# Performance work log

Hardware: AMD Instinct MI355X
Metric: run time of the kernel (lower is better)

Reference implementation:

```python
import jax, jax.numpy as jnp
import numpy as np

STRIDES = (8, 16, 32, 64, 128)
HS = (192, 96, 48, 24, 12)
NUM_CLASSES = 15
NUM_THETA = 18
B = 16
SCORE_THR = 0.05
IOU_THR = 0.3
MAX_DET = 1000


def setup_inputs() -> dict:
    key = jax.random.key(0)
    ks = jax.random.split(key, 20)
    inp = {}
    i = 0
    for name, c in (("cls", NUM_CLASSES), ("reg", 5), ("tc", NUM_THETA), ("tr", 1)):
        for l, h in enumerate(HS):
            inp[f"{name}_l{l}"] = jax.random.normal(ks[i], (B, c, h, h), dtype=jnp.float32)
            i += 1
    return inp


def _coords():
    # FCOS-style location centers per level, concatenated: [N, 2] (x, y)
    outs = []
    for h, s in zip(HS, STRIDES):
        c1d = jnp.arange(h, dtype=jnp.float32) * s + s // 2
        yy, xx = jnp.meshgrid(c1d, c1d, indexing="ij")
        outs.append(jnp.stack([xx.ravel(), yy.ravel()], axis=-1))
    return jnp.concatenate(outs, axis=0)


def _flatten(levels):
    # list of [B,C,h,w] -> [B, sum(h*w), C]  (permute to NHWC then reshape, as in torch)
    b = levels[0].shape[0]
    return jnp.concatenate(
        [jnp.transpose(t, (0, 2, 3, 1)).reshape(b, -1, t.shape[1]) for t in levels], axis=1
    )


def _pairwise_iou(boxes):
    # boxes [M,5] (x1,y1,x2,y2,theta); axis-aligned IoU on first 4 coords
    x1, y1, x2, y2 = boxes[:, 0], boxes[:, 1], boxes[:, 2], boxes[:, 3]
    area = jnp.clip(x2 - x1, 0.0) * jnp.clip(y2 - y1, 0.0)
    iw = jnp.clip(jnp.minimum(x2[:, None], x2[None, :]) - jnp.maximum(x1[:, None], x1[None, :]), 0.0)
    ih = jnp.clip(jnp.minimum(y2[:, None], y2[None, :]) - jnp.maximum(y1[:, None], y1[None, :]), 0.0)
    inter = iw * ih
    union = area[:, None] + area[None, :] - inter
    return inter / jnp.maximum(union, 1e-8)


def _nms_keep(boxes, valid, iou_thr):
    # greedy NMS over score-sorted boxes; returns bool keep mask [M]
    m = boxes.shape[0]
    iou = _pairwise_iou(boxes)
    idx = jnp.arange(m)

    def body(i, keep):
        sup = keep[i] & (iou[i] > iou_thr) & (idx > i)
        return keep & ~sup

    return jax.lax.fori_loop(0, m, body, valid)


def _forward(cls_levels, reg_levels, tc_levels, tr_levels):
    coords = _coords()  # [N,2]

    cls_preds = jax.nn.sigmoid(_flatten(cls_levels))          # [B,N,15]
    cls_scores = jnp.max(cls_preds, axis=-1)                   # [B,N]
    cls_classes = jnp.argmax(cls_preds, axis=-1) + 1           # [B,N]

    tc_preds = jax.nn.sigmoid(_flatten(tc_levels))             # [B,N,18]
    theta_c = (jnp.argmax(tc_preds, axis=-1) + 1)[..., None].astype(jnp.float32)  # [B,N,1]
    tr_lo = _flatten(tr_levels)                                # [B,N,1]
    theta = theta_c * 10.0 + tr_lo                             # [B,N,1]

    # reg: scale ltrb channels (0:4) by stride per level, keep angle channel raw
    reg_parts = []
    for t, s in zip(reg_levels, STRIDES):
        r = jnp.transpose(t, (0, 2, 3, 1)).reshape(t.shape[0], -1, 5)
        reg_parts.append(jnp.concatenate([r[..., :4] * float(s), r[..., 4:]], axis=-1))
    reg = jnp.concatenate(reg_parts, axis=1)                   # [B,N,5]

    x1y1 = coords[None, :, :] - reg[..., :2]
    x2y2 = coords[None, :, :] + reg[..., 2:4]
    boxes = jnp.concatenate([x1y1, x2y2, theta], axis=-1)      # [B,N,5]

    max_num = min(MAX_DET, cls_scores.shape[-1])
    top_scores, top_idx = jax.lax.top_k(cls_scores, max_num)   # sorted desc
    boxes_topk = jnp.take_along_axis(boxes, top_idx[..., None], axis=1)   # [B,M,5]
    classes_topk = jnp.take_along_axis(cls_classes, top_idx, axis=1)      # [B,M]

    valid = top_scores >= SCORE_THR
    keep = jax.vmap(lambda b, v: _nms_keep(b, v, IOU_THR))(boxes_topk, valid)  # [B,M] bool

    scores_post = top_scores * keep
    classes_post = classes_topk * keep
    boxes_post = boxes_topk * keep[..., None]
    return scores_post, classes_post, boxes_post


def reference(cls_l0, cls_l1, cls_l2, cls_l3, cls_l4,
              reg_l0, reg_l1, reg_l2, reg_l3, reg_l4,
              tc_l0, tc_l1, tc_l2, tc_l3, tc_l4,
              tr_l0, tr_l1, tr_l2, tr_l3, tr_l4):
    return _forward(
        [cls_l0, cls_l1, cls_l2, cls_l3, cls_l4],
        [reg_l0, reg_l1, reg_l2, reg_l3, reg_l4],
        [tc_l0, tc_l1, tc_l2, tc_l3, tc_l4],
        [tr_l0, tr_l1, tr_l2, tr_l3, tr_l4],
    )
```

## Files before the change

kernel.cpp:

```cpp
#include <hip/hip_runtime.h>
#include <stdint.h>

#define NCLS   15
#define NTH    18
#define BATCH  16
#define NANCH  49104
#define KTOP   1000
#define NWORDS 16
#define NBIN   32768
#define BSHIFT 15
#define CAND   2048

__device__ __forceinline__ float sigmoidf(float x) {
    return 1.0f / (1.0f + expf(-x));
}

__device__ __forceinline__ void levelOf(int i, int& lvl, int& h, int& s, int& pos) {
    if (i < 36864)      { lvl = 0; h = 192; s = 8;   pos = i; }
    else if (i < 46080) { lvl = 1; h = 96;  s = 16;  pos = i - 36864; }
    else if (i < 48384) { lvl = 2; h = 48;  s = 32;  pos = i - 46080; }
    else if (i < 48960) { lvl = 3; h = 24;  s = 64;  pos = i - 48384; }
    else                { lvl = 4; h = 12;  s = 128; pos = i - 48960; }
}

__device__ __forceinline__ unsigned long long shfl_u64(unsigned long long v, int src) {
    int lo = __shfl((int)(unsigned int)(v & 0xFFFFFFFFull), src);
    int hi = __shfl((int)(unsigned int)(v >> 32), src);
    return ((unsigned long long)(unsigned int)hi << 32) | (unsigned long long)(unsigned int)lo;
}

__device__ __forceinline__ void atomicOr64Shared(unsigned long long* p, unsigned long long v) {
    unsigned int* q = (unsigned int*)p;
    unsigned int lo = (unsigned int)v;
    unsigned int hi = (unsigned int)(v >> 32);
    if (lo) atomicOr(q, lo);
    if (hi) atomicOr(q + 1, hi);
}

__global__ __launch_bounds__(256) void k_scores(
    const float* __restrict__ c0, const float* __restrict__ c1,
    const float* __restrict__ c2, const float* __restrict__ c3,
    const float* __restrict__ c4,
    float* __restrict__ scores, unsigned int* __restrict__ hist)
{
    __shared__ unsigned int lh[NBIN / 2];
    const int b = blockIdx.y;
    for (int i = threadIdx.x; i < NBIN / 2; i += 256) lh[i] = 0u;
    __syncthreads();

    #pragma unroll
    for (int r = 0; r < 2; ++r) {
        int f4 = blockIdx.x * 512 + r * 256 + threadIdx.x;
        if (f4 < NANCH / 4) {
            int i = f4 * 4;
            int lvl, h, s, pos;
            levelOf(i, lvl, h, s, pos);
            int hh = h * h;
            const float* cp = (lvl == 0) ? c0 : (lvl == 1) ? c1 : (lvl == 2) ? c2
                              : (lvl == 3) ? c3 : c4;
            const float* base = cp + (size_t)b * NCLS * hh + pos;
            float4 mx = make_float4(-1e30f, -1e30f, -1e30f, -1e30f);
            #pragma unroll
            for (int c = 0; c < NCLS; ++c) {
                float4 v = *(const float4*)(base + (size_t)c * hh);
                mx.x = fmaxf(mx.x, v.x); mx.y = fmaxf(mx.y, v.y);
                mx.z = fmaxf(mx.z, v.z); mx.w = fmaxf(mx.w, v.w);
            }
            float4 sc = make_float4(sigmoidf(mx.x), sigmoidf(mx.y),
                                    sigmoidf(mx.z), sigmoidf(mx.w));
            *(float4*)(scores + (size_t)b * NANCH + i) = sc;
            unsigned int bin;
            bin = __float_as_uint(sc.x) >> BSHIFT;
            atomicAdd(&lh[bin >> 1], 1u << ((bin & 1) << 4));
            bin = __float_as_uint(sc.y) >> BSHIFT;
            atomicAdd(&lh[bin >> 1], 1u << ((bin & 1) << 4));
            bin = __float_as_uint(sc.z) >> BSHIFT;
            atomicAdd(&lh[bin >> 1], 1u << ((bin & 1) << 4));
            bin = __float_as_uint(sc.w) >> BSHIFT;
            atomicAdd(&lh[bin >> 1], 1u << ((bin & 1) << 4));
        }
    }
    __syncthreads();

    unsigned int* hb = hist + (size_t)b * NBIN;
    for (int wd = threadIdx.x; wd < NBIN / 2; wd += 256) {
        unsigned int v = lh[wd];
        if (v) {
            unsigned int lo = v & 0xFFFFu, hi = v >> 16;
            if (lo) atomicAdd(&hb[wd * 2], lo);
            if (hi) atomicAdd(&hb[wd * 2 + 1], hi);
        }
    }
}

__global__ __launch_bounds__(256) void k_findT(
    const unsigned int* __restrict__ hist, int* __restrict__ tbin)
{
    int b = blockIdx.x;
    int tid = threadIdx.x;
    const unsigned int* hb = hist + (size_t)b * NBIN;
    __shared__ unsigned int sc[256];
    __shared__ unsigned int fsc[128];
    __shared__ int s_c, s_t;

    unsigned int s = 0;
    const uint4* hv = (const uint4*)(hb + (size_t)tid * 128);
    #pragma unroll 8
    for (int k = 0; k < 32; ++k) {
        uint4 v = hv[k];
        s += v.x + v.y + v.z + v.w;
    }
    sc[tid] = s;
    if (tid == 0) { s_c = 0; s_t = 0; }
    __syncthreads();
    for (int d = 1; d < 256; d <<= 1) {
        unsigned int add = (tid + d < 256) ? sc[tid + d] : 0;
        __syncthreads();
        sc[tid] += add;
        __syncthreads();
    }
    if (sc[tid] >= (unsigned int)KTOP && (tid == 255 || sc[tid + 1] < (unsigned int)KTOP))
        s_c = tid;
    __syncthreads();
    int c = s_c;
    unsigned int hi = (c < 255) ? sc[c + 1] : 0;
    if (tid < 128) fsc[tid] = hb[c * 128 + tid];
    __syncthreads();
    for (int d = 1; d < 128; d <<= 1) {
        unsigned int add = (tid < 128 && tid + d < 128) ? fsc[tid + d] : 0;
        __syncthreads();
        if (tid < 128) fsc[tid] += add;
        __syncthreads();
    }
    if (tid < 128 && hi + fsc[tid] >= (unsigned int)KTOP &&
        (tid == 127 || hi + fsc[tid + 1] < (unsigned int)KTOP))
        s_t = tid;
    __syncthreads();
    if (tid == 0) tbin[b] = c * 128 + s_t;
}

__global__ __launch_bounds__(256) void k_compact(
    const float* __restrict__ scores, const int* __restrict__ tbin,
    int* __restrict__ cnt, unsigned long long* __restrict__ cand)
{
    const int b = blockIdx.y;
    const int t4 = blockIdx.x * 256 + threadIdx.x;
    __shared__ int lcnt;
    __shared__ int lbase;
    if (threadIdx.x == 0) lcnt = 0;
    __syncthreads();

    const int T = tbin[b];
    const bool in = (t4 < NANCH / 4);
    float4 v = make_float4(0.f, 0.f, 0.f, 0.f);
    if (in) v = *(const float4*)(scores + (size_t)b * NANCH + 4 * (size_t)t4);
    unsigned int bits[4] = { __float_as_uint(v.x), __float_as_uint(v.y),
                             __float_as_uint(v.z), __float_as_uint(v.w) };
    int rank[4];
    #pragma unroll
    for (int k = 0; k < 4; ++k) {
        bool pass = in && ((int)(bits[k] >> BSHIFT) >= T);
        rank[k] = pass ? atomicAdd(&lcnt, 1) : -1;
    }
    __syncthreads();
    if (threadIdx.x == 0) lbase = atomicAdd(&cnt[b * 16], lcnt);
    __syncthreads();
    const int base = lbase;
    #pragma unroll
    for (int k = 0; k < 4; ++k) {
        if (rank[k] >= 0) {
            int p = base + rank[k];
            if (p < CAND) {
                unsigned int idx = 4u * (unsigned int)t4 + (unsigned int)k;
                cand[(size_t)b * CAND + p] =
                    ((unsigned long long)bits[k] << 32) |
                    (unsigned long long)(0xFFFFFFFFu - idx);
            }
        }
    }
}

__global__ __launch_bounds__(1024) void k_sortk(
    const unsigned long long* __restrict__ cand, const int* __restrict__ cnt,
    float* __restrict__ tsc, int* __restrict__ tix)
{
    int b = blockIdx.x;
    int tid = threadIdx.x;
    __shared__ unsigned long long keys[CAND];
    int n = cnt[b * 16]; if (n > CAND) n = CAND;
    for (int i = tid; i < CAND; i += 1024)
        keys[i] = (i < n) ? cand[(size_t)b * CAND + i] : 0ull;
    __syncthreads();
    for (int sz = 2; sz <= CAND; sz <<= 1) {
        for (int st = sz >> 1; st > 0; st >>= 1) {
            for (int i = tid; i < CAND; i += 1024) {
                int j = i ^ st;
                if (j > i) {
                    unsigned long long a = keys[i], c = keys[j];
                    bool desc = ((i & sz) == 0);
                    if (desc ? (a < c) : (a > c)) { keys[i] = c; keys[j] = a; }
                }
            }
            __syncthreads();
        }
    }
    if (tid < KTOP) {
        unsigned long long key = keys[tid];
        tsc[b * KTOP + tid] = __uint_as_float((unsigned int)(key >> 32));
        tix[b * KTOP + tid] = (int)(0xFFFFFFFFu - (unsigned int)(key & 0xFFFFFFFFull));
    }
}

__global__ __launch_bounds__(256) void k_decode(
    const float* __restrict__ c0, const float* __restrict__ c1,
    const float* __restrict__ c2, const float* __restrict__ c3,
    const float* __restrict__ c4,
    const float* __restrict__ r0, const float* __restrict__ r1,
    const float* __restrict__ r2, const float* __restrict__ r3,
    const float* __restrict__ r4,
    const float* __restrict__ t0, const float* __restrict__ t1,
    const float* __restrict__ t2, const float* __restrict__ t3,
    const float* __restrict__ t4,
    const float* __restrict__ q0, const float* __restrict__ q1,
    const float* __restrict__ q2, const float* __restrict__ q3,
    const float* __restrict__ q4,
    const int* __restrict__ tix, float* __restrict__ boxes, int* __restrict__ clstop)
{
    int g = blockIdx.x * 256 + threadIdx.x;
    if (g >= BATCH * KTOP) return;
    int b = g / KTOP;
    int idx = tix[g];
    int lvl, h, s, pos;
    levelOf(idx, lvl, h, s, pos);
    int y = pos / h, x = pos - y * h;
    int hh = h * h;
    const float* cp = (lvl == 0) ? c0 : (lvl == 1) ? c1 : (lvl == 2) ? c2 : (lvl == 3) ? c3 : c4;
    const float* rp = (lvl == 0) ? r0 : (lvl == 1) ? r1 : (lvl == 2) ? r2 : (lvl == 3) ? r3 : r4;
    const float* tp = (lvl == 0) ? t0 : (lvl == 1) ? t1 : (lvl == 2) ? t2 : (lvl == 3) ? t3 : t4;
    const float* qp = (lvl == 0) ? q0 : (lvl == 1) ? q1 : (lvl == 2) ? q2 : (lvl == 3) ? q3 : q4;
    int off = y * h + x;

    const float* cb = cp + (size_t)b * NCLS * hh + off;
    float bestc = -1e30f; int bc = 0;
    #pragma unroll
    for (int c = 0; c < NCLS; ++c) {
        float v = sigmoidf(cb[(size_t)c * hh]);
        if (v > bestc) { bestc = v; bc = c; }
    }
    clstop[g] = bc + 1;

    const float* tb = tp + (size_t)b * NTH * hh + off;
    float best = -1e30f; int bt = 0;
    #pragma unroll
    for (int c = 0; c < NTH; ++c) {
        float v = sigmoidf(tb[(size_t)c * hh]);
        if (v > best) { best = v; bt = c; }
    }
    float theta = (float)(bt + 1) * 10.0f + qp[(size_t)b * hh + off];

    const float* rb = rp + (size_t)b * 5 * hh + off;
    float fs = (float)s;
    float rr0 = rb[0] * fs;
    float rr1 = rb[(size_t)hh] * fs;
    float rr2 = rb[(size_t)2 * hh] * fs;
    float rr3 = rb[(size_t)3 * hh] * fs;
    float cx = (float)(x * s + (s >> 1));
    float cy = (float)(y * s + (s >> 1));
    float* op = boxes + (size_t)g * 5;
    op[0] = cx - rr0;
    op[1] = cy - rr1;
    op[2] = cx + rr2;
    op[3] = cy + rr3;
    op[4] = theta;
}

__global__ __launch_bounds__(256) void k_mask(
    const float* __restrict__ boxes, unsigned long long* __restrict__ mask)
{
    const int b = blockIdx.x;
    const int by = blockIdx.y;
    __shared__ float bx1[1024], by1[1024], bx2[1024], by2[1024], bar[1024];
    for (int r = threadIdx.x; r < 1024; r += 256) {
        float x1 = 0.f, y1 = 0.f, x2 = 0.f, y2 = 0.f;
        if (r < KTOP) {
            const float* p = boxes + ((size_t)(b * KTOP + r)) * 5;
            x1 = p[0]; y1 = p[1]; x2 = p[2]; y2 = p[3];
        }
        bx1[r] = x1; by1[r] = y1; bx2[r] = x2; by2[r] = y2;
        bar[r] = fmaxf(x2 - x1, 0.0f) * fmaxf(y2 - y1, 0.0f);
    }
    __syncthreads();

    const int l  = threadIdx.x & 63;
    const int wv = threadIdx.x >> 6;
    const int i  = (by << 6) + l;
    const float x1 = bx1[i], y1 = by1[i], x2 = bx2[i], y2 = by2[i], ai = bar[i];

    for (int w = by + wv; w < NWORDS; w += 4) {
        const int j0 = w << 6;
        unsigned long long m = 0ull;
        #pragma unroll 8
        for (int jj = 0; jj < 64; ++jj) {
            const int j = j0 + jj;
            float iw = fminf(x2, bx2[j]) - fmaxf(x1, bx1[j]);
            iw = fmaxf(iw, 0.0f);
            float ih = fminf(y2, by2[j]) - fmaxf(y1, by1[j]);
            ih = fmaxf(ih, 0.0f);
            float inter = iw * ih;
            float u = ai + bar[j] - inter;
            float iou = inter / fmaxf(u, 1e-8f);
            unsigned long long bit = (iou > 0.3f && j > i) ? 1ull : 0ull;
            m |= bit << jj;
        }
        mask[(((size_t)b * 1024 + i) << 4) + w] = m;
    }
}

#define LOADROW(R, W) do {                                                          \
    const ulonglong2* rp2 = (const ulonglong2*)(mask +                              \
        (((size_t)b * 1024 + ((W) << 6) + l) << 4));                                \
    _Pragma("unroll")                                                               \
    for (int p = 0; p < 8; ++p) {                                                   \
        ulonglong2 v = rp2[p]; R[2 * p] = v.x; R[2 * p + 1] = v.y;                  \
    }                                                                               \
} while (0)

#define PROC(W, R) do {                                                             \
    const unsigned long long rowword = R[W];                                        \
    unsigned long long zr = __ballot(rowword == 0ull);                              \
    unsigned long long remw = sremv[W];                                             \
    unsigned long long pend = vw[W] & ~remw;                                        \
    unsigned long long keptm = 0ull;                                                \
    while (pend) {                                                                  \
        unsigned long long nzp = pend & ~zr;                                        \
        if (!nzp) { keptm |= pend; break; }                                         \
        int jj = __builtin_ctzll(nzp);                                              \
        unsigned long long low = (1ull << jj); low = (low << 1) - 1ull;             \
        keptm |= pend & low;                                                        \
        remw |= shfl_u64(rowword, jj);                                              \
        pend &= ~low; pend &= ~remw;                                                \
    }                                                                               \
    if (l == 0) skeep[W] = keptm;                                                   \
    if ((keptm >> l) & 1ull) {                                                      \
        _Pragma("unroll")                                                           \
        for (int w2 = (W) + 1; w2 < NWORDS; ++w2)                                   \
            if (R[w2]) atomicOr64Shared(&sremv[w2], R[w2]);                         \
    }                                                                               \
} while (0)

__global__ __launch_bounds__(64) void k_nms(
    const unsigned long long* __restrict__ mask,
    const float* __restrict__ tsc, const int* __restrict__ clstop,
    const float* __restrict__ boxes, float* __restrict__ out)
{
    const int b = blockIdx.x;
    const int l = threadIdx.x;
    __shared__ unsigned long long sremv[NWORDS];
    __shared__ unsigned long long skeep[NWORDS];

    if (l < NWORDS) sremv[l] = 0ull;

    unsigned long long vw[NWORDS];
    #pragma unroll
    for (int w = 0; w < NWORDS; ++w) {
        int i = (w << 6) + l;
        bool v = (i < KTOP) && (tsc[b * KTOP + i] >= 0.05f);
        vw[w] = __ballot(v);
    }

    unsigned long long rowA[NWORDS], rowB[NWORDS];
    LOADROW(rowA, 0);
    LOADROW(rowB, 1);   PROC(0, rowA);
    LOADROW(rowA, 2);   PROC(1, rowB);
    LOADROW(rowB, 3);   PROC(2, rowA);
    LOADROW(rowA, 4);   PROC(3, rowB);
    LOADROW(rowB, 5);   PROC(4, rowA);
    LOADROW(rowA, 6);   PROC(5, rowB);
    LOADROW(rowB, 7);   PROC(6, rowA);
    LOADROW(rowA, 8);   PROC(7, rowB);
    LOADROW(rowB, 9);   PROC(8, rowA);
    LOADROW(rowA, 10);  PROC(9, rowB);
    LOADROW(rowB, 11);  PROC(10, rowA);
    LOADROW(rowA, 12);  PROC(11, rowB);
    LOADROW(rowB, 13);  PROC(12, rowA);
    LOADROW(rowA, 14);  PROC(13, rowB);
    LOADROW(rowB, 15);  PROC(14, rowA);
    PROC(15, rowB);

    #pragma unroll
    for (int w = 0; w < NWORDS; ++w) {
        int i = (w << 6) + l;
        if (i < KTOP) {
            int g = b * KTOP + i;
            float fk = (float)((skeep[w] >> l) & 1ull);
            out[g] = tsc[g] * fk;
            out[BATCH * KTOP + g] = (float)clstop[g] * fk;
            const float* bp = boxes + (size_t)g * 5;
            float* op = out + 2 * BATCH * KTOP + (size_t)g * 5;
            op[0] = bp[0] * fk;
            op[1] = bp[1] * fk;
            op[2] = bp[2] * fk;
            op[3] = bp[3] * fk;
            op[4] = bp[4] * fk;
        }
    }
}

extern "C" void kernel_launch(void* const* d_in, const int* in_sizes, int n_in,
                              void* d_out, int out_size, void* d_ws, size_t ws_size,
                              hipStream_t stream) {
    const float* c0 = (const float*)d_in[0];
    const float* c1 = (const float*)d_in[1];
    const float* c2 = (const float*)d_in[2];
    const float* c3 = (const float*)d_in[3];
    const float* c4 = (const float*)d_in[4];
    const float* r0 = (const float*)d_in[5];
    const float* r1 = (const float*)d_in[6];
    const float* r2 = (const float*)d_in[7];
    const float* r3 = (const float*)d_in[8];
    const float* r4 = (const float*)d_in[9];
    const float* t0 = (const float*)d_in[10];
    const float* t1 = (const float*)d_in[11];
    const float* t2 = (const float*)d_in[12];
    const float* t3 = (const float*)d_in[13];
    const float* t4 = (const float*)d_in[14];
    const float* q0 = (const float*)d_in[15];
    const float* q1 = (const float*)d_in[16];
    const float* q2 = (const float*)d_in[17];
    const float* q3 = (const float*)d_in[18];
    const float* q4 = (const float*)d_in[19];

    char* ws = (char*)d_ws;
    float*              scores  = (float*)(ws + 0);
    float*              tsc     = (float*)(ws + 3142656);
    int*                tix     = (int*)(ws + 3206656);
    float*              boxes   = (float*)(ws + 3270656);
    unsigned long long* cand    = (unsigned long long*)(ws + 3270656);
    int*                clstop  = (int*)(ws + 3590656);
    unsigned long long* mask    = (unsigned long long*)(ws + 3654656);
    unsigned int*       hist    = (unsigned int*)(ws + 3654656);
    int*                tcnt    = (int*)(ws + 5751808);
    int*                tbin    = (int*)(ws + 5752832);
    float*              out     = (float*)d_out;

    hipMemsetAsync(ws + 3654656, 0, 2098176, stream);

    k_scores<<<dim3(24, BATCH), 256, 0, stream>>>(
        c0, c1, c2, c3, c4, scores, hist);
    k_findT<<<BATCH, 256, 0, stream>>>(hist, tbin);
    k_compact<<<dim3(48, BATCH), 256, 0, stream>>>(scores, tbin, tcnt, cand);
    k_sortk<<<BATCH, 1024, 0, stream>>>(cand, tcnt, tsc, tix);
    k_decode<<<(BATCH * KTOP + 255) / 256, 256, 0, stream>>>(
        c0, c1, c2, c3, c4,
        r0, r1, r2, r3, r4, t0, t1, t2, t3, t4, q0, q1, q2, q3, q4,
        tix, boxes, clstop);
    k_mask<<<dim3(BATCH, 16), 256, 0, stream>>>(boxes, mask);
    k_nms<<<BATCH, 64, 0, stream>>>(mask, tsc, clstop, boxes, out);
}
```

Baseline: 123.3 us.

## Fuse histogram, threshold search, compaction and sort into one per-batch kernel

The global histogram, threshold-finding, compaction and sort kernels are merged into a single per-batch 1024-thread kernel. It builds the histogram in shared memory, finds the threshold bin with a block scan plus a wave shuffle, compacts candidates into shared memory and bitonic-sorts them there. This removes the 2 MB memset, the global atomics and three kernel launches, and k_scores becomes a flat grid with no histogram work. The cost is that only 16 blocks handle the histogram and compaction, each reading its batch's scores twice, so GPU occupancy drops for that phase.

```diff
diff --git a/kernel.cpp b/kernel.cpp
--- a/kernel.cpp
+++ b/kernel.cpp
@@ -41,169 +41,139 @@
     const float* __restrict__ c0, const float* __restrict__ c1,
     const float* __restrict__ c2, const float* __restrict__ c3,
     const float* __restrict__ c4,
-    float* __restrict__ scores, unsigned int* __restrict__ hist)
+    float* __restrict__ scores)
 {
-    __shared__ unsigned int lh[NBIN / 2];
-    const int b = blockIdx.y;
-    for (int i = threadIdx.x; i < NBIN / 2; i += 256) lh[i] = 0u;
-    __syncthreads();
-
-    #pragma unroll
-    for (int r = 0; r < 2; ++r) {
-        int f4 = blockIdx.x * 512 + r * 256 + threadIdx.x;
-        if (f4 < NANCH / 4) {
-            int i = f4 * 4;
-            int lvl, h, s, pos;
-            levelOf(i, lvl, h, s, pos);
-            int hh = h * h;
-            const float* cp = (lvl == 0) ? c0 : (lvl == 1) ? c1 : (lvl == 2) ? c2
-                              : (lvl == 3) ? c3 : c4;
-            const float* base = cp + (size_t)b * NCLS * hh + pos;
-            float4 mx = make_float4(-1e30f, -1e30f, -1e30f, -1e30f);
-            #pragma unroll
-            for (int c = 0; c < NCLS; ++c) {
-                float4 v = *(const float4*)(base + (size_t)c * hh);
-                mx.x = fmaxf(mx.x, v.x); mx.y = fmaxf(mx.y, v.y);
-                mx.z = fmaxf(mx.z, v.z); mx.w = fmaxf(mx.w, v.w);
-            }
-            float4 sc = make_float4(sigmoidf(mx.x), sigmoidf(mx.y),
-                                    sigmoidf(mx.z), sigmoidf(mx.w));
-            *(float4*)(scores + (size_t)b * NANCH + i) = sc;
-            unsigned int bin;
-            bin = __float_as_uint(sc.x) >> BSHIFT;
-            atomicAdd(&lh[bin >> 1], 1u << ((bin & 1) << 4));
-            bin = __float_as_uint(sc.y) >> BSHIFT;
-            atomicAdd(&lh[bin >> 1], 1u << ((bin & 1) << 4));
-            bin = __float_as_uint(sc.z) >> BSHIFT;
-            atomicAdd(&lh[bin >> 1], 1u << ((bin & 1) << 4));
-            bin = __float_as_uint(sc.w) >> BSHIFT;
-            atomicAdd(&lh[bin >> 1], 1u << ((bin & 1) << 4));
-        }
-    }
-    __syncthreads();
-
-    unsigned int* hb = hist + (size_t)b * NBIN;
-    for (int wd = threadIdx.x; wd < NBIN / 2; wd += 256) {
-        unsigned int v = lh[wd];
-        if (v) {
-            unsigned int lo = v & 0xFFFFu, hi = v >> 16;
-            if (lo) atomicAdd(&hb[wd * 2], lo);
-            if (hi) atomicAdd(&hb[wd * 2 + 1], hi);
-        }
-    }
-}
-
-__global__ __launch_bounds__(256) void k_findT(
-    const unsigned int* __restrict__ hist, int* __restrict__ tbin)
-{
-    int b = blockIdx.x;
-    int tid = threadIdx.x;
-    const unsigned int* hb = hist + (size_t)b * NBIN;
-    __shared__ unsigned int sc[256];
-    __shared__ unsigned int fsc[128];
-    __shared__ int s_c, s_t;
-
-    unsigned int s = 0;
-    const uint4* hv = (const uint4*)(hb + (size_t)tid * 128);
-    #pragma unroll 8
-    for (int k = 0; k < 32; ++k) {
-        uint4 v = hv[k];
-        s += v.x + v.y + v.z + v.w;
-    }
-    sc[tid] = s;
-    if (tid == 0) { s_c = 0; s_t = 0; }
-    __syncthreads();
-    for (int d = 1; d < 256; d <<= 1) {
-        unsigned int add = (tid + d < 256) ? sc[tid + d] : 0;
-        __syncthreads();
-        sc[tid] += add;
-        __syncthreads();
-    }
-    if (sc[tid] >= (unsigned int)KTOP && (tid == 255 || sc[tid + 1] < (unsigned int)KTOP))
-        s_c = tid;
-    __syncthreads();
-    int c = s_c;
-    unsigned int hi = (c < 255) ? sc[c + 1] : 0;
-    if (tid < 128) fsc[tid] = hb[c * 128 + tid];
-    __syncthreads();
-    for (int d = 1; d < 128; d <<= 1) {
-        unsigned int add = (tid < 128 && tid + d < 128) ? fsc[tid + d] : 0;
-        __syncthreads();
-        if (tid < 128) fsc[tid] += add;
-        __syncthreads();
-    }
-    if (tid < 128 && hi + fsc[tid] >= (unsigned int)KTOP &&
-        (tid == 127 || hi + fsc[tid + 1] < (unsigned int)KTOP))
-        s_t = tid;
-    __syncthreads();
-    if (tid == 0) tbin[b] = c * 128 + s_t;
-}
-
-__global__ __launch_bounds__(256) void k_compact(
-    const float* __restrict__ scores, const int* __restrict__ tbin,
-    int* __restrict__ cnt, unsigned long long* __restrict__ cand)
-{
-    const int b = blockIdx.y;
-    const int t4 = blockIdx.x * 256 + threadIdx.x;
-    __shared__ int lcnt;
-    __shared__ int lbase;
-    if (threadIdx.x == 0) lcnt = 0;
-    __syncthreads();
-
-    const int T = tbin[b];
-    const bool in = (t4 < NANCH / 4);
-    float4 v = make_float4(0.f, 0.f, 0.f, 0.f);
-    if (in) v = *(const float4*)(scores + (size_t)b * NANCH + 4 * (size_t)t4);
-    unsigned int bits[4] = { __float_as_uint(v.x), __float_as_uint(v.y),
-                             __float_as_uint(v.z), __float_as_uint(v.w) };
-    int rank[4];
-    #pragma unroll
-    for (int k = 0; k < 4; ++k) {
-        bool pass = in && ((int)(bits[k] >> BSHIFT) >= T);
-        rank[k] = pass ? atomicAdd(&lcnt, 1) : -1;
-    }
-    __syncthreads();
-    if (threadIdx.x == 0) lbase = atomicAdd(&cnt[b * 16], lcnt);
-    __syncthreads();
-    const int base = lbase;
-    #pragma unroll
-    for (int k = 0; k < 4; ++k) {
-        if (rank[k] >= 0) {
-            int p = base + rank[k];
-            if (p < CAND) {
-                unsigned int idx = 4u * (unsigned int)t4 + (unsigned int)k;
-                cand[(size_t)b * CAND + p] =
-                    ((unsigned long long)bits[k] << 32) |
-                    (unsigned long long)(0xFFFFFFFFu - idx);
-            }
-        }
-    }
-}
-
-__global__ __launch_bounds__(1024) void k_sortk(
-    const unsigned long long* __restrict__ cand, const int* __restrict__ cnt,
+    int g4 = blockIdx.x * 256 + threadIdx.x;
+    if (g4 >= BATCH * NANCH / 4) return;
+    int g = g4 * 4;
+    int b = g / NANCH;
+    int i = g - b * NANCH;
+    int lvl, h, s, pos;
+    levelOf(i, lvl, h, s, pos);
+    int hh = h * h;
+    const float* cp = (lvl == 0) ? c0 : (lvl == 1) ? c1 : (lvl == 2) ? c2
+                      : (lvl == 3) ? c3 : c4;
+    const float* base = cp + (size_t)b * NCLS * hh + pos;
+    float4 mx = make_float4(-1e30f, -1e30f, -1e30f, -1e30f);
+    #pragma unroll
+    for (int c = 0; c < NCLS; ++c) {
+        float4 v = *(const float4*)(base + (size_t)c * hh);
+        mx.x = fmaxf(mx.x, v.x); mx.y = fmaxf(mx.y, v.y);
+        mx.z = fmaxf(mx.z, v.z); mx.w = fmaxf(mx.w, v.w);
+    }
+    float4 sc = make_float4(sigmoidf(mx.x), sigmoidf(mx.y),
+                            sigmoidf(mx.z), sigmoidf(mx.w));
+    *(float4*)(scores + g) = sc;
+}
+
+__global__ __launch_bounds__(1024) void k_select(
+    const float* __restrict__ scores,
     float* __restrict__ tsc, int* __restrict__ tix)
 {
-    int b = blockIdx.x;
-    int tid = threadIdx.x;
-    __shared__ unsigned long long keys[CAND];
-    int n = cnt[b * 16]; if (n > CAND) n = CAND;
-    for (int i = tid; i < CAND; i += 1024)
-        keys[i] = (i < n) ? cand[(size_t)b * CAND + i] : 0ull;
-    __syncthreads();
+    const int b   = blockIdx.x;
+    const int tid = threadIdx.x;
+    __shared__ unsigned long long smem[NBIN / 4];
+    __shared__ unsigned int csum[1024];
+    __shared__ int s_c, s_T, s_cnt;
+    unsigned int* lh = (unsigned int*)smem;
+    unsigned long long* keys = smem;
+
+    for (int i = tid; i < NBIN / 2; i += 1024) lh[i] = 0u;
+    if (tid == 0) { s_c = 0; s_T = 0; s_cnt = 0; }
+    __syncthreads();
+
+    const float4* sv = (const float4*)(scores + (size_t)b * NANCH);
+    for (int f4 = tid; f4 < NANCH / 4; f4 += 1024) {
+        float4 v = sv[f4];
+        unsigned int bin;
+        bin = __float_as_uint(v.x) >> BSHIFT;
+        atomicAdd(&lh[bin >> 1], 1u << ((bin & 1) << 4));
+        bin = __float_as_uint(v.y) >> BSHIFT;
+        atomicAdd(&lh[bin >> 1], 1u << ((bin & 1) << 4));
+        bin = __float_as_uint(v.z) >> BSHIFT;
+        atomicAdd(&lh[bin >> 1], 1u << ((bin & 1) << 4));
+        bin = __float_as_uint(v.w) >> BSHIFT;
+        atomicAdd(&lh[bin >> 1], 1u << ((bin & 1) << 4));
+    }
+    __syncthreads();
+
+    unsigned int s = 0;
+    #pragma unroll
+    for (int k = 0; k < 16; ++k) {
+        unsigned int w = lh[tid * 16 + k];
+        s += (w & 0xFFFFu) + (w >> 16);
+    }
+    csum[tid] = s;
+    __syncthreads();
+    for (int d = 1; d < 1024; d <<= 1) {
+        unsigned int add = (tid + d < 1024) ? csum[tid + d] : 0u;
+        __syncthreads();
+        csum[tid] += add;
+        __syncthreads();
+    }
+    if (csum[tid] >= (unsigned)KTOP &&
+        (tid == 1023 || csum[tid + 1] < (unsigned)KTOP))
+        s_c = tid;
+    __syncthreads();
+    const int c = s_c;
+    const unsigned int hi = (c < 1023) ? csum[c + 1] : 0u;
+
+    if (tid < 64) {
+        unsigned int cnt = 0;
+        if (tid < 32) {
+            int bin = c * 32 + tid;
+            cnt = (lh[bin >> 1] >> ((bin & 1) << 4)) & 0xFFFFu;
+        }
+        unsigned int suf = cnt;
+        #pragma unroll
+        for (int d = 1; d < 32; d <<= 1) {
+            unsigned int o = __shfl_down(suf, d);
+            if (tid + d < 32) suf += o;
+        }
+        unsigned int nxt = __shfl_down(suf, 1);
+        if (tid < 32) {
+            if (hi + suf >= (unsigned)KTOP &&
+                (tid == 31 || hi + nxt < (unsigned)KTOP))
+                s_T = c * 32 + tid;
+        }
+    }
+    __syncthreads();
+    const int T = s_T;
+
+    keys[tid] = 0ull; keys[tid + 1024] = 0ull;
+    __syncthreads();
+    for (int f4 = tid; f4 < NANCH / 4; f4 += 1024) {
+        float4 v = sv[f4];
+        unsigned int bits[4] = { __float_as_uint(v.x), __float_as_uint(v.y),
+                                 __float_as_uint(v.z), __float_as_uint(v.w) };
+        #pragma unroll
+        for (int k = 0; k < 4; ++k) {
+            if ((int)(bits[k] >> BSHIFT) >= T) {
+                int p = atomicAdd(&s_cnt, 1);
+                if (p < CAND) {
+                    unsigned int idx = 4u * (unsigned int)f4 + (unsigned int)k;
+                    keys[p] = ((unsigned long long)bits[k] << 32) |
+                              (unsigned long long)(0xFFFFFFFFu - idx);
+                }
+            }
+        }
+    }
+    __syncthreads();
+
     for (int sz = 2; sz <= CAND; sz <<= 1) {
         for (int st = sz >> 1; st > 0; st >>= 1) {
             for (int i = tid; i < CAND; i += 1024) {
                 int j = i ^ st;
                 if (j > i) {
-                    unsigned long long a = keys[i], c = keys[j];
+                    unsigned long long a = keys[i], cc = keys[j];
                     bool desc = ((i & sz) == 0);
-                    if (desc ? (a < c) : (a > c)) { keys[i] = c; keys[j] = a; }
+                    if (desc ? (a < cc) : (a > cc)) { keys[i] = cc; keys[j] = a; }
                 }
             }
             __syncthreads();
         }
     }
+
     if (tid < KTOP) {
         unsigned long long key = keys[tid];
         tsc[b * KTOP + tid] = __uint_as_float((unsigned int)(key >> 32));
@@ -435,21 +405,13 @@
     float*              tsc     = (float*)(ws + 3142656);
     int*                tix     = (int*)(ws + 3206656);
     float*              boxes   = (float*)(ws + 3270656);
-    unsigned long long* cand    = (unsigned long long*)(ws + 3270656);
     int*                clstop  = (int*)(ws + 3590656);
     unsigned long long* mask    = (unsigned long long*)(ws + 3654656);
-    unsigned int*       hist    = (unsigned int*)(ws + 3654656);
-    int*                tcnt    = (int*)(ws + 5751808);
-    int*                tbin    = (int*)(ws + 5752832);
     float*              out     = (float*)d_out;
 
-    hipMemsetAsync(ws + 3654656, 0, 2098176, stream);
-
-    k_scores<<<dim3(24, BATCH), 256, 0, stream>>>(
-        c0, c1, c2, c3, c4, scores, hist);
-    k_findT<<<BATCH, 256, 0, stream>>>(hist, tbin);
-    k_compact<<<dim3(48, BATCH), 256, 0, stream>>>(scores, tbin, tcnt, cand);
-    k_sortk<<<BATCH, 1024, 0, stream>>>(cand, tcnt, tsc, tix);
+    k_scores<<<(BATCH * NANCH / 4 + 255) / 256, 256, 0, stream>>>(
+        c0, c1, c2, c3, c4, scores);
+    k_select<<<BATCH, 1024, 0, stream>>>(scores, tsc, tix);
     k_decode<<<(BATCH * KTOP + 255) / 256, 256, 0, stream>>>(
         c0, c1, c2, c3, c4,
         r0, r1, r2, r3, r4, t0, t1, t2, t3, t4, q0, q1, q2, q3, q4,
```

After: 112.1 us. 9.1% less time.
